# Kernel optimization log

Measured on AMD Instinct MI355X. Metric: run time of the kernel, lower is better.

Reference implementation:

```python
import jax, jax.numpy as jnp
import numpy as np

B, S, H = 4, 2048, 512
I = 1024  # intermediate_dim
E = 8     # num_experts
K = 2     # top_k


def setup_inputs() -> dict:
    key = jax.random.key(0)
    k1, k2, k3, k4 = jax.random.split(key, 4)
    x = jax.random.normal(k1, (B, S, H), dtype=jnp.float32)
    expert_indices = jax.random.randint(k2, (B, S, K), 0, E, dtype=jnp.int32)
    # parameters: init.normal_(std=0.02)
    w13 = 0.02 * jax.random.normal(k3, (E, H, 2 * I), dtype=jnp.float32)
    w2 = 0.02 * jax.random.normal(k4, (E, I, H), dtype=jnp.float32)
    return {"x": x, "expert_indices": expert_indices, "w13": w13, "w2": w2}


def reference(x, expert_indices, w13, w2):
    # x: (B,S,H); expert_indices: (B,S,K); w13: (E,H,2I); w2: (E,I,H)
    # Same math as torch's per-token weight gather + matmul, expressed as
    # dense all-expert GEMM followed by per-token expert selection.
    h13_all = jnp.einsum('bsh,ehd->bsed', x, w13)          # (B,S,E,2I)
    h13 = jnp.take_along_axis(h13_all, expert_indices[..., None], axis=2)  # (B,S,K,2I)
    gate, up = jnp.split(h13, 2, axis=-1)                   # each (B,S,K,I)
    h_inter = jax.nn.silu(gate) * up                        # (B,S,K,I)
    out_all = jnp.einsum('bski,eih->bskeh', h_inter, w2)    # (B,S,K,E,H)
    out = jnp.take_along_axis(out_all, expert_indices[..., None, None], axis=3)
    return out.squeeze(3)                                   # (B,S,K,H)
```

## Files before the change

kernel.cpp:

```cpp
#include <hip/hip_runtime.h>


#define H_DIM 512
#define I_DIM 1024
#define E_NUM 8
#define P_PAIRS 16384
#define CAP P_PAIRS
#define MAX_TILES 136

#define PREP_TW13 2048
#define PREP_TW2 1024
#define PREP_CVT 2048
#define PREP_ROUTE 64
#define PREP_BLOCKS (PREP_TW13 + PREP_TW2 + PREP_CVT + PREP_ROUTE)

typedef _Float16 half8 __attribute__((ext_vector_type(8)));
typedef float f32x4 __attribute__((ext_vector_type(4)));
typedef unsigned int u32;
typedef const __attribute__((address_space(1))) u32* gas_t;
typedef __attribute__((address_space(3))) u32* las_t;

__device__ __forceinline__ void glds16(const void* g, void* l) {
  __builtin_amdgcn_global_load_lds((gas_t)g, (las_t)l, 16, 0, 0);
}

__device__ __forceinline__ bool tile_decode(const int* counts, int ty, int& e,
                                            int& m0, int& ne, int& rb) {
  int base = 0;
  rb = 0;
  for (e = 0; e < E_NUM; ++e) {
    ne = counts[e];
    const int nt = (ne + 127) >> 7;
    if (ty < base + nt) { m0 = (ty - base) << 7; return true; }
    base += nt;
    rb += ne;
  }
  return false;
}

__global__ __launch_bounds__(256) void prep_k(
    const float* __restrict__ x, const int* __restrict__ idx,
    const float* __restrict__ w13, const float* __restrict__ w2,
    int* __restrict__ counts, int* __restrict__ lists,
    _Float16* __restrict__ xh, _Float16* __restrict__ w13t,
    _Float16* __restrict__ w2t) {
  __shared__ __align__(16) _Float16 tile[64][72];
  const int b = blockIdx.x;
  const int tid = threadIdx.x;

  if (b < PREP_TW13 + PREP_TW2) {
    const float* src;
    _Float16* dst;
    int R, C, c0, r0;
    if (b < PREP_TW13) {
      R = H_DIM; C = 2 * I_DIM;
      const int e = b >> 8;
      c0 = (b & 31) * 64;
      r0 = ((b >> 5) & 7) * 64;
      src = w13 + (size_t)e * R * C;
      dst = w13t + (size_t)e * C * R;
    } else {
      const int l = b - PREP_TW13;
      R = I_DIM; C = H_DIM;
      const int e = l >> 7;
      c0 = (l & 7) * 64;
      r0 = ((l >> 3) & 15) * 64;
      src = w2 + (size_t)e * R * C;
      dst = w2t + (size_t)e * C * R;
    }
    {
      const int r = tid >> 4;
      const int c4 = (tid & 15) * 4;
      for (int pass = 0; pass < 4; ++pass) {
        f32x4 v = *(const f32x4*)(src + (size_t)(r0 + pass * 16 + r) * C + c0 + c4);
        for (int j = 0; j < 4; ++j) tile[c4 + j][pass * 16 + r] = (_Float16)v[j];
      }
    }
    __syncthreads();
    {
      const int c = tid >> 3;
      const int r8 = (tid & 7) * 8;
      for (int pass = 0; pass < 2; ++pass) {
        half8 h = *(const half8*)&tile[pass * 32 + c][r8];
        *(half8*)(dst + (size_t)(c0 + pass * 32 + c) * R + r0 + r8) = h;
      }
    }
  } else if (b < PREP_TW13 + PREP_TW2 + PREP_CVT) {
    const int l = b - (PREP_TW13 + PREP_TW2);
    const size_t i = ((size_t)l * 256 + tid) * 8;
    f32x4 v0 = *(const f32x4*)(x + i);
    f32x4 v1 = *(const f32x4*)(x + i + 4);
    half8 h;
    for (int j = 0; j < 4; ++j) { h[j] = (_Float16)v0[j]; h[j + 4] = (_Float16)v1[j]; }
    *(half8*)(xh + i) = h;
  } else {
    int* lcnt = (int*)&tile[0][0];
    int* lbase = lcnt + E_NUM;
    const int l = b - (PREP_TW13 + PREP_TW2 + PREP_CVT);
    if (tid < E_NUM) lcnt[tid] = 0;
    __syncthreads();
    const int p = l * 256 + tid;
    const int e = idx[p];
    const int r = atomicAdd(&lcnt[e], 1);
    __syncthreads();
    if (tid < E_NUM) lbase[tid] = atomicAdd(&counts[tid], lcnt[tid]);
    __syncthreads();
    lists[e * CAP + lbase[e] + r] = p;
  }
}

__global__ __launch_bounds__(256) void gemm1_k(
    const _Float16* __restrict__ xh, const _Float16* __restrict__ w13t,
    const int* __restrict__ counts, const int* __restrict__ lists,
    _Float16* __restrict__ h_ws) {
  int e, m0, ne, rb;
  if (!tile_decode(counts, blockIdx.y, e, m0, ne, rb)) return;
  const int n0 = blockIdx.x * 64;

  __shared__ int rows[128];
  __shared__ __align__(16) _Float16 As[2][128 * 32];
  __shared__ __align__(16) _Float16 Bgs[2][64 * 32];
  __shared__ __align__(16) _Float16 Bus[2][64 * 32];

  const int tid = threadIdx.x;
  if (tid < 128) {
    const int m = m0 + tid;
    rows[tid] = (m < ne) ? lists[e * CAP + m] : -1;
  }
  __syncthreads();

  const int sr = tid >> 2;
  const int s4 = tid & 3;
  const int segoff = ((s4 ^ ((sr >> 1) & 3)) * 8);
  const int pa0 = rows[sr];
  const int pa1 = rows[64 + sr];
  const int t0 = (pa0 >= 0) ? (pa0 >> 1) : 0;
  const int t1 = (pa1 >= 0) ? (pa1 >> 1) : 0;
  const _Float16* ga0 = xh + (size_t)t0 * H_DIM + segoff;
  const _Float16* ga1 = xh + (size_t)t1 * H_DIM + segoff;
  const _Float16* gbg = w13t + ((size_t)e * 2 * I_DIM + n0 + sr) * H_DIM + segoff;
  const _Float16* gbu = gbg + (size_t)I_DIM * H_DIM;
  const int la0 = sr * 32 + s4 * 8;
  const int la1 = (64 + sr) * 32 + s4 * 8;
  const int lb = sr * 32 + s4 * 8;

  const int lane = tid & 63;
  const int wid = tid >> 6;
  const int wm = wid & 1;
  const int wn = wid >> 1;
  const int fm = lane & 15;
  const int q = lane >> 4;
  int aoff[4], boff[2];
  for (int mi = 0; mi < 4; ++mi) {
    const int rA = wm * 64 + mi * 16 + fm;
    aoff[mi] = rA * 32 + ((q ^ ((rA >> 1) & 3)) * 8);
  }
  for (int ni = 0; ni < 2; ++ni) {
    const int cB = wn * 32 + ni * 16 + fm;
    boff[ni] = cB * 32 + ((q ^ ((cB >> 1) & 3)) * 8);
  }

  f32x4 accg[4][2] = {};
  f32x4 accu[4][2] = {};

#define G1_STAGE(buf, k0)                    \
  do {                                       \
    glds16(ga0 + (k0), &As[buf][la0]);       \
    glds16(ga1 + (k0), &As[buf][la1]);       \
    glds16(gbg + (k0), &Bgs[buf][lb]);       \
    glds16(gbu + (k0), &Bus[buf][lb]);       \
  } while (0)

#define G1_COMPUTE(buf)                                                         \
  do {                                                                          \
    half8 af[4], bg[2], bu[2];                                                  \
    for (int mi = 0; mi < 4; ++mi) af[mi] = *(const half8*)&As[buf][aoff[mi]];  \
    for (int ni = 0; ni < 2; ++ni) {                                            \
      bg[ni] = *(const half8*)&Bgs[buf][boff[ni]];                              \
      bu[ni] = *(const half8*)&Bus[buf][boff[ni]];                              \
    }                                                                           \
    for (int mi = 0; mi < 4; ++mi)                                              \
      for (int ni = 0; ni < 2; ++ni) {                                          \
        accg[mi][ni] = __builtin_amdgcn_mfma_f32_16x16x32_f16(                  \
            af[mi], bg[ni], accg[mi][ni], 0, 0, 0);                             \
        accu[mi][ni] = __builtin_amdgcn_mfma_f32_16x16x32_f16(                  \
            af[mi], bu[ni], accu[mi][ni], 0, 0, 0);                             \
      }                                                                         \
  } while (0)

  G1_STAGE(0, 0);
  __syncthreads();
  for (int k0 = 0; k0 < H_DIM; k0 += 64) {
    G1_STAGE(1, k0 + 32);
    G1_COMPUTE(0);
    __syncthreads();
    if (k0 + 64 < H_DIM) G1_STAGE(0, k0 + 64);
    G1_COMPUTE(1);
    __syncthreads();
  }
#undef G1_STAGE
#undef G1_COMPUTE

  for (int mi = 0; mi < 4; ++mi)
    for (int r = 0; r < 4; ++r) {
      const int mrow = wm * 64 + mi * 16 + q * 4 + r;
      if (m0 + mrow >= ne) continue;
      _Float16* hrow = h_ws + (size_t)(rb + m0 + mrow) * I_DIM + n0;
      for (int ni = 0; ni < 2; ++ni) {
        const int c = wn * 32 + ni * 16 + fm;
        const float g = accg[mi][ni][r];
        const float u = accu[mi][ni][r];
        hrow[c] = (_Float16)(g / (1.0f + __expf(-g)) * u);
      }
    }
}

__global__ __launch_bounds__(256) void gemm2_k(
    const _Float16* __restrict__ h_ws, const _Float16* __restrict__ w2t,
    const int* __restrict__ counts, const int* __restrict__ lists,
    float* __restrict__ out) {
  int e, m0, ne, rb;
  if (!tile_decode(counts, blockIdx.x, e, m0, ne, rb)) return;
  const int n0 = blockIdx.y * 64;

  __shared__ int rows[128];
  __shared__ __align__(16) _Float16 As[2][128 * 64];
  __shared__ __align__(16) _Float16 Bs[2][64 * 64];

  const int tid = threadIdx.x;
  if (tid < 128) {
    const int m = m0 + tid;
    rows[tid] = (m < ne) ? lists[e * CAP + m] : -1;
  }

  const int s8 = tid & 7;
  const int sr8 = tid >> 3;
  const int sw = ((s8 ^ (sr8 & 7)) * 8);
  const _Float16* gA[4];
  int lA[4];
  for (int pa = 0; pa < 4; ++pa) {
    const int m = pa * 32 + sr8;
    int grow = rb + m0 + m;
    if (grow > P_PAIRS - 1) grow = P_PAIRS - 1;
    gA[pa] = h_ws + (size_t)grow * I_DIM + sw;
    lA[pa] = m * 64 + s8 * 8;
  }
  const _Float16* gB[2];
  int lB[2];
  for (int pb = 0; pb < 2; ++pb) {
    const int n = pb * 32 + sr8;
    gB[pb] = w2t + ((size_t)e * H_DIM + n0 + n) * I_DIM + sw;
    lB[pb] = n * 64 + s8 * 8;
  }

  const int lane = tid & 63;
  const int wid = tid >> 6;
  const int wm = wid & 1;
  const int wn = wid >> 1;
  const int fm = lane & 15;
  const int q = lane >> 4;
  int aoff[2][4], boff[2][2];
  for (int ks = 0; ks < 2; ++ks) {
    for (int mi = 0; mi < 4; ++mi) {
      const int rA = wm * 64 + mi * 16 + fm;
      aoff[ks][mi] = rA * 64 + (((ks * 4 + q) ^ (rA & 7)) * 8);
    }
    for (int ni = 0; ni < 2; ++ni) {
      const int cB = wn * 32 + ni * 16 + fm;
      boff[ks][ni] = cB * 64 + (((ks * 4 + q) ^ (cB & 7)) * 8);
    }
  }

  f32x4 acc[4][2] = {};

#define G2_STAGE(buf, k0)                                  \
  do {                                                     \
    for (int pa = 0; pa < 4; ++pa)                         \
      glds16(gA[pa] + (k0), &As[buf][lA[pa]]);             \
    for (int pb = 0; pb < 2; ++pb)                         \
      glds16(gB[pb] + (k0), &Bs[buf][lB[pb]]);             \
  } while (0)

#define G2_COMPUTE(buf)                                                          \
  do {                                                                           \
    for (int ks = 0; ks < 2; ++ks) {                                             \
      half8 af[4], bf[2];                                                        \
      for (int mi = 0; mi < 4; ++mi)                                             \
        af[mi] = *(const half8*)&As[buf][aoff[ks][mi]];                          \
      for (int ni = 0; ni < 2; ++ni)                                             \
        bf[ni] = *(const half8*)&Bs[buf][boff[ks][ni]];                          \
      for (int mi = 0; mi < 4; ++mi)                                             \
        for (int ni = 0; ni < 2; ++ni)                                           \
          acc[mi][ni] = __builtin_amdgcn_mfma_f32_16x16x32_f16(                  \
              af[mi], bf[ni], acc[mi][ni], 0, 0, 0);                             \
    }                                                                            \
  } while (0)

  G2_STAGE(0, 0);
  __syncthreads();
  for (int k0 = 0; k0 < I_DIM; k0 += 128) {
    G2_STAGE(1, k0 + 64);
    G2_COMPUTE(0);
    __syncthreads();
    if (k0 + 128 < I_DIM) G2_STAGE(0, k0 + 128);
    G2_COMPUTE(1);
    __syncthreads();
  }
#undef G2_STAGE
#undef G2_COMPUTE

  for (int mi = 0; mi < 4; ++mi)
    for (int r = 0; r < 4; ++r) {
      const int mrow = wm * 64 + mi * 16 + q * 4 + r;
      const int p = rows[mrow];
      if (p < 0) continue;
      float* orow = out + (size_t)p * H_DIM + n0;
      for (int ni = 0; ni < 2; ++ni)
        orow[wn * 32 + ni * 16 + fm] = acc[mi][ni][r];
    }
}

extern "C" void kernel_launch(void* const* d_in, const int* in_sizes, int n_in,
                              void* d_out, int out_size, void* d_ws, size_t ws_size,
                              hipStream_t stream) {
  const float* x = (const float*)d_in[0];
  const int* idx = (const int*)d_in[1];
  const float* w13 = (const float*)d_in[2];
  const float* w2 = (const float*)d_in[3];

  char* ws = (char*)d_ws;
  int* counts = (int*)ws;
  int* lists = (int*)(ws + 2048);
  const size_t OFF_XH = 2048 + (size_t)E_NUM * CAP * 4;
  const size_t OFF_W13T = OFF_XH + (size_t)P_PAIRS / 2 * H_DIM * 2;
  const size_t OFF_W2T = OFF_W13T + (size_t)E_NUM * 2 * I_DIM * H_DIM * 2;
  const size_t OFF_H = OFF_W2T + (size_t)E_NUM * H_DIM * I_DIM * 2;
  _Float16* xh = (_Float16*)(ws + OFF_XH);
  _Float16* w13t = (_Float16*)(ws + OFF_W13T);
  _Float16* w2t = (_Float16*)(ws + OFF_W2T);
  _Float16* h_ws = (_Float16*)(ws + OFF_H);

  hipMemsetAsync(d_ws, 0, 128, stream);
  prep_k<<<dim3(PREP_BLOCKS), 256, 0, stream>>>(x, idx, w13, w2, counts, lists,
                                                xh, w13t, w2t);
  gemm1_k<<<dim3(I_DIM / 64, MAX_TILES), 256, 0, stream>>>(
      xh, w13t, counts, lists, h_ws);
  gemm2_k<<<dim3(MAX_TILES, H_DIM / 64), 256, 0, stream>>>(
      h_ws, w2t, counts, lists, (float*)d_out);
}
```

Before: 206.6 us.

## Drop gemm1 double buffering and vectorize prep transpose LDS writes

The gemm1 kernel moves from a double-buffered LDS pipeline to a single buffer, loading each 32-wide k slice and then computing on it, separated by two barriers per step. This halves LDS use per block, which may allow more resident blocks, but it gives up the overlap between global-to-LDS loads and MFMA work. In the prep transpose, each thread now loads four rows and writes packed half4 values into a tile with padding 68 instead of 72, cutting the number of LDS store instructions. The tile change also alters the bank-conflict pattern and LDS read alignment.

```diff
diff --git a/kernel.cpp b/kernel.cpp
--- a/kernel.cpp
+++ b/kernel.cpp
@@ -15,6 +15,7 @@
 #define PREP_BLOCKS (PREP_TW13 + PREP_TW2 + PREP_CVT + PREP_ROUTE)
 
 typedef _Float16 half8 __attribute__((ext_vector_type(8)));
+typedef _Float16 half4 __attribute__((ext_vector_type(4)));
 typedef float f32x4 __attribute__((ext_vector_type(4)));
 typedef unsigned int u32;
 typedef const __attribute__((address_space(1))) u32* gas_t;
@@ -44,7 +45,7 @@
     int* __restrict__ counts, int* __restrict__ lists,
     _Float16* __restrict__ xh, _Float16* __restrict__ w13t,
     _Float16* __restrict__ w2t) {
-  __shared__ __align__(16) _Float16 tile[64][72];
+  __shared__ __align__(16) _Float16 tile[64][68];
   const int b = blockIdx.x;
   const int tid = threadIdx.x;
 
@@ -69,11 +70,15 @@
       dst = w2t + (size_t)e * C * R;
     }
     {
-      const int r = tid >> 4;
       const int c4 = (tid & 15) * 4;
-      for (int pass = 0; pass < 4; ++pass) {
-        f32x4 v = *(const f32x4*)(src + (size_t)(r0 + pass * 16 + r) * C + c0 + c4);
-        for (int j = 0; j < 4; ++j) tile[c4 + j][pass * 16 + r] = (_Float16)v[j];
+      const int r4 = (tid >> 4) * 4;
+      f32x4 v[4];
+      for (int i = 0; i < 4; ++i)
+        v[i] = *(const f32x4*)(src + (size_t)(r0 + r4 + i) * C + c0 + c4);
+      for (int j = 0; j < 4; ++j) {
+        half4 hv = {(_Float16)v[0][j], (_Float16)v[1][j],
+                    (_Float16)v[2][j], (_Float16)v[3][j]};
+        *(half4*)&tile[c4 + j][r4] = hv;
       }
     }
     __syncthreads();
@@ -81,8 +86,11 @@
       const int c = tid >> 3;
       const int r8 = (tid & 7) * 8;
       for (int pass = 0; pass < 2; ++pass) {
-        half8 h = *(const half8*)&tile[pass * 32 + c][r8];
-        *(half8*)(dst + (size_t)(c0 + pass * 32 + c) * R + r0 + r8) = h;
+        const int col = pass * 32 + c;
+        half4 lo = *(const half4*)&tile[col][r8];
+        half4 hi = *(const half4*)&tile[col][r8 + 4];
+        half8 h = {lo[0], lo[1], lo[2], lo[3], hi[0], hi[1], hi[2], hi[3]};
+        *(half8*)(dst + (size_t)(c0 + col) * R + r0 + r8) = h;
       }
     }
   } else if (b < PREP_TW13 + PREP_TW2 + PREP_CVT) {
@@ -118,9 +126,9 @@
   const int n0 = blockIdx.x * 64;
 
   __shared__ int rows[128];
-  __shared__ __align__(16) _Float16 As[2][128 * 32];
-  __shared__ __align__(16) _Float16 Bgs[2][64 * 32];
-  __shared__ __align__(16) _Float16 Bus[2][64 * 32];
+  __shared__ __align__(16) _Float16 As[128 * 32];
+  __shared__ __align__(16) _Float16 Bgs[64 * 32];
+  __shared__ __align__(16) _Float16 Bus[64 * 32];
 
   const int tid = threadIdx.x;
   if (tid < 128) {
@@ -140,9 +148,10 @@
   const _Float16* ga1 = xh + (size_t)t1 * H_DIM + segoff;
   const _Float16* gbg = w13t + ((size_t)e * 2 * I_DIM + n0 + sr) * H_DIM + segoff;
   const _Float16* gbu = gbg + (size_t)I_DIM * H_DIM;
-  const int la0 = sr * 32 + s4 * 8;
-  const int la1 = (64 + sr) * 32 + s4 * 8;
-  const int lb = sr * 32 + s4 * 8;
+  _Float16* la0 = As + sr * 32 + s4 * 8;
+  _Float16* la1 = As + (64 + sr) * 32 + s4 * 8;
+  _Float16* lbg = Bgs + sr * 32 + s4 * 8;
+  _Float16* lbu = Bus + sr * 32 + s4 * 8;
 
   const int lane = tid & 63;
   const int wid = tid >> 6;
@@ -163,43 +172,26 @@
   f32x4 accg[4][2] = {};
   f32x4 accu[4][2] = {};
 
-#define G1_STAGE(buf, k0)                    \
-  do {                                       \
-    glds16(ga0 + (k0), &As[buf][la0]);       \
-    glds16(ga1 + (k0), &As[buf][la1]);       \
-    glds16(gbg + (k0), &Bgs[buf][lb]);       \
-    glds16(gbu + (k0), &Bus[buf][lb]);       \
-  } while (0)
-
-#define G1_COMPUTE(buf)                                                         \
-  do {                                                                          \
-    half8 af[4], bg[2], bu[2];                                                  \
-    for (int mi = 0; mi < 4; ++mi) af[mi] = *(const half8*)&As[buf][aoff[mi]];  \
-    for (int ni = 0; ni < 2; ++ni) {                                            \
-      bg[ni] = *(const half8*)&Bgs[buf][boff[ni]];                              \
-      bu[ni] = *(const half8*)&Bus[buf][boff[ni]];                              \
-    }                                                                           \
-    for (int mi = 0; mi < 4; ++mi)                                              \
-      for (int ni = 0; ni < 2; ++ni) {                                          \
-        accg[mi][ni] = __builtin_amdgcn_mfma_f32_16x16x32_f16(                  \
-            af[mi], bg[ni], accg[mi][ni], 0, 0, 0);                             \
-        accu[mi][ni] = __builtin_amdgcn_mfma_f32_16x16x32_f16(                  \
-            af[mi], bu[ni], accu[mi][ni], 0, 0, 0);                             \
-      }                                                                         \
-  } while (0)
-
-  G1_STAGE(0, 0);
-  __syncthreads();
-  for (int k0 = 0; k0 < H_DIM; k0 += 64) {
-    G1_STAGE(1, k0 + 32);
-    G1_COMPUTE(0);
-    __syncthreads();
-    if (k0 + 64 < H_DIM) G1_STAGE(0, k0 + 64);
-    G1_COMPUTE(1);
-    __syncthreads();
-  }
-#undef G1_STAGE
-#undef G1_COMPUTE
+  for (int k0 = 0; k0 < H_DIM; k0 += 32) {
+    glds16(ga0 + k0, la0);
+    glds16(ga1 + k0, la1);
+    glds16(gbg + k0, lbg);
+    glds16(gbu + k0, lbu);
+    __syncthreads();
+
+    half8 af[4], bg[2], bu[2];
+    for (int mi = 0; mi < 4; ++mi) af[mi] = *(const half8*)&As[aoff[mi]];
+    for (int ni = 0; ni < 2; ++ni) {
+      bg[ni] = *(const half8*)&Bgs[boff[ni]];
+      bu[ni] = *(const half8*)&Bus[boff[ni]];
+    }
+    for (int mi = 0; mi < 4; ++mi)
+      for (int ni = 0; ni < 2; ++ni) {
+        accg[mi][ni] = __builtin_amdgcn_mfma_f32_16x16x32_f16(af[mi], bg[ni], accg[mi][ni], 0, 0, 0);
+        accu[mi][ni] = __builtin_amdgcn_mfma_f32_16x16x32_f16(af[mi], bu[ni], accu[mi][ni], 0, 0, 0);
+      }
+    __syncthreads();
+  }
 
   for (int mi = 0; mi < 4; ++mi)
     for (int r = 0; r < 4; ++r) {
```

After: 201.1 us. 2.6% less time.
